# Kernel tuning notes

Measured on AMD Instinct MI355X. Metric: run time of the kernel, lower is better.

The kernel has to match this reference:

```python
import jax, jax.numpy as jnp
import numpy as np


def setup_inputs() -> dict:
    key = jax.random.key(0)
    k_xyz, k_w1, k_b1, k_w2, k_b2 = jax.random.split(key, 5)
    B, N = 2, 1024
    D_MODEL, N_HEADS = 128, 8
    HID = D_MODEL // 2
    # Kaiming-ish init scale for the tiny MLP weights
    return {
        "xyz": jax.random.normal(k_xyz, (B, 3, N), dtype=jnp.float32),
        "W1": jax.random.normal(k_w1, (3, HID), dtype=jnp.float32) * (1.0 / np.sqrt(3.0)),
        "b1": jax.random.normal(k_b1, (HID,), dtype=jnp.float32) * 0.01,
        "W2": jax.random.normal(k_w2, (HID, N_HEADS), dtype=jnp.float32) * (1.0 / np.sqrt(HID)),
        "b2": jax.random.normal(k_b2, (N_HEADS,), dtype=jnp.float32) * 0.01,
    }


def reference(xyz, W1, b1, W2, b2):
    # xyz: [B, 3, N] -> [B, N, 3]
    pts = jnp.transpose(xyz, (0, 2, 1))
    # pairwise relative positions: rel[b, i, j, :] = pts[b, j] - pts[b, i]
    # (matches xyz.unsqueeze(1) - xyz.unsqueeze(2) in torch)
    rel = pts[:, None, :, :] - pts[:, :, None, :]          # [B, N, N, 3]
    h = jax.nn.relu(jnp.einsum("bijc,ch->bijh", rel, W1) + b1)  # [B, N, N, HID]
    bias = jnp.einsum("bijh,hk->bijk", h, W2) + b2         # [B, N, N, H]
    # permute(0, 3, 1, 2) -> [B, H, N, N]
    return jnp.transpose(bias, (0, 3, 1, 2))
```

## Files before the change

kernel.cpp:

```cpp
#include <hip/hip_runtime.h>

#define HID   64
#define NHD   8
#define IT    8
#define IGRP  4
#define WAVES 8
#define JTW   32
#define JT    (WAVES*JTW)

typedef _Float16 f16x8 __attribute__((ext_vector_type(8)));
typedef float    f32x4 __attribute__((ext_vector_type(4)));

__global__ __launch_bounds__(WAVES * 64, 4) void relposenc_occ2(
    const float* __restrict__ xyz, const float* __restrict__ W1,
    const float* __restrict__ b1,  const float* __restrict__ W2,
    const float* __restrict__ b2,  float* __restrict__ out, int N) {

  __shared__ float    sW1b1[4][HID];
  __shared__ _Float16 sU[IT][HID];

  const int tid  = threadIdx.x;
  const int wave = tid >> 6;
  const int lane = tid & 63;
  const int col  = lane & 15;
  const int hgrp = lane >> 4;
  const int b    = blockIdx.z;
  const int i0   = blockIdx.y * IT;
  const int j0   = blockIdx.x * JT + wave * JTW;

  const float* xb = xyz + (size_t)b * 3 * N;

  if (tid < 4 * HID) {
    int r = tid >> 6, h = tid & 63;
    sW1b1[r][h] = (r < 3) ? W1[r * HID + h] : b1[h];
  }
  if (tid < IT * HID) {
    int ii = tid >> 6, h = tid & 63;
    int i  = i0 + ii;
    float u = fmaf(xb[i], W1[h],
              fmaf(xb[N + i], W1[HID + h],
                   xb[2 * N + i] * W1[2 * HID + h]));
    sU[ii][h] = (_Float16)u;
  }

  f16x8 aLo[2], aHi[2];
  #pragma unroll
  for (int kb = 0; kb < 2; ++kb)
    #pragma unroll
    for (int e = 0; e < 8; ++e) {
      int h = kb * 32 + hgrp * 8 + e;
      aLo[kb][e] = (_Float16)((col < NHD)  ? W2[h * NHD + col]       : 0.f);
      aHi[kb][e] = (_Float16)((col >= NHD) ? W2[h * NHD + (col - 8)] : 0.f);
    }
  float b2v[4];
  #pragma unroll
  for (int r = 0; r < 4; ++r) b2v[r] = b2[((hgrp & 1) << 2) + r];

  __syncthreads();

  f16x8 aj[2][2];
  #pragma unroll
  for (int t = 0; t < 2; ++t) {
    int j = j0 + t * 16 + col;
    float x0 = xb[j], x1 = xb[N + j], x2 = xb[2 * N + j];
    #pragma unroll
    for (int kb = 0; kb < 2; ++kb)
      #pragma unroll
      for (int e = 0; e < 8; ++e) {
        int h = kb * 32 + hgrp * 8 + e;
        float v = fmaf(x0, sW1b1[0][h],
                  fmaf(x1, sW1b1[1][h],
                  fmaf(x2, sW1b1[2][h], sW1b1[3][h])));
        aj[t][kb][e] = (_Float16)v;
      }
  }

  const size_t jj = (size_t)j0 + col + ((size_t)(lane >> 5) << 4);
  const int kbase = (hgrp & 1) << 2;
  const size_t baseOff = ((size_t)(b * NHD + kbase) * N + i0) * N + jj;
  const size_t plane = (size_t)N * N;

  const f16x8 z = {0, 0, 0, 0, 0, 0, 0, 0};

  for (int ig = 0; ig < IT; ig += IGRP) {
    f32x4 vals[IGRP];

    #pragma unroll
    for (int q = 0; q < IGRP; ++q) {
      f16x8 u0 = *(const f16x8*)&sU[ig + q][hgrp * 8];
      f16x8 u1 = *(const f16x8*)&sU[ig + q][32 + hgrp * 8];

      f16x8 d00 = __builtin_elementwise_max(aj[0][0] - u0, z);
      f16x8 d01 = __builtin_elementwise_max(aj[0][1] - u1, z);
      f16x8 d10 = __builtin_elementwise_max(aj[1][0] - u0, z);
      f16x8 d11 = __builtin_elementwise_max(aj[1][1] - u1, z);

      f32x4 cA = {b2v[0], b2v[1], b2v[2], b2v[3]};
      f32x4 cB = {0.f, 0.f, 0.f, 0.f};
      cA = __builtin_amdgcn_mfma_f32_16x16x32_f16(aLo[0], d00, cA, 0, 0, 0);
      cA = __builtin_amdgcn_mfma_f32_16x16x32_f16(aLo[1], d01, cA, 0, 0, 0);
      cB = __builtin_amdgcn_mfma_f32_16x16x32_f16(aHi[0], d10, cB, 0, 0, 0);
      cB = __builtin_amdgcn_mfma_f32_16x16x32_f16(aHi[1], d11, cB, 0, 0, 0);
      vals[q] = cA + cB;
    }

    #pragma unroll
    for (int r = 0; r < 4; ++r) {
      const size_t po = baseOff + (size_t)r * plane + (size_t)ig * N;
      #pragma unroll
      for (int q = 0; q < IGRP; ++q)
        out[po + (size_t)q * N] = vals[q][r];
    }
  }
}

extern "C" void kernel_launch(void* const* d_in, const int* in_sizes, int n_in,
                              void* d_out, int out_size, void* d_ws, size_t ws_size,
                              hipStream_t stream) {
  const float* xyz = (const float*)d_in[0];
  const float* W1  = (const float*)d_in[1];
  const float* b1  = (const float*)d_in[2];
  const float* W2  = (const float*)d_in[3];
  const float* b2  = (const float*)d_in[4];
  float* out = (float*)d_out;

  const long long in0 = in_sizes[0];
  const int N = (int)((3LL * (long long)out_size) / (8LL * in0));
  const int B = (int)(in0 / (3LL * N));

  dim3 grid(N / JT, N / IT, B);
  relposenc_occ2<<<grid, WAVES * 64, 0, stream>>>(xyz, W1, b1, W2, b2, out, N);
}
```

Before: 25.45 us.

## Precompute per-point W1 projections in a prep kernel and shrink main tiles

Adds a prep kernel that computes the per-point first-layer projections u and u+b1 as fp16, plus a transposed fp16 W2, and stores them in workspace. The main kernel then loads these vectors directly instead of recomputing them per block through shared memory and a barrier. Block size drops from 8 to 4 waves and the i-tile from 8 to 4 rows, giving more, smaller blocks. The cost is a second kernel launch and a global round-trip for the precomputed data.

Result: slower. 32.33 us (+27.0%).

```diff
diff --git a/kernel.cpp b/kernel.cpp
--- a/kernel.cpp
+++ b/kernel.cpp
@@ -2,22 +2,52 @@
 
 #define HID   64
 #define NHD   8
-#define IT    8
-#define IGRP  4
-#define WAVES 8
+#define IT    4
+#define WAVES 4
 #define JTW   32
 #define JT    (WAVES*JTW)
 
 typedef _Float16 f16x8 __attribute__((ext_vector_type(8)));
 typedef float    f32x4 __attribute__((ext_vector_type(4)));
 
-__global__ __launch_bounds__(WAVES * 64, 4) void relposenc_occ2(
+__global__ __launch_bounds__(256) void relpos_prep(
     const float* __restrict__ xyz, const float* __restrict__ W1,
     const float* __restrict__ b1,  const float* __restrict__ W2,
-    const float* __restrict__ b2,  float* __restrict__ out, int N) {
+    _Float16* __restrict__ u_all, _Float16* __restrict__ a_all,
+    _Float16* __restrict__ w2t, int N, int BN) {
+  const int tid = threadIdx.x;
+  if (blockIdx.x == 0) {
+    for (int t = tid; t < NHD * HID; t += 256) {
+      int k = t >> 6, h = t & 63;
+      w2t[k * HID + h] = (_Float16)W2[h * NHD + k];
+    }
+  }
+  int g = blockIdx.x * 256 + tid;
+  if (g >= BN) return;
+  int b = g / N, n = g - b * N;
+  const float* xb = xyz + (size_t)b * 3 * N;
+  float x0 = xb[n], x1 = xb[N + n], x2 = xb[2 * N + n];
+  _Float16* up = u_all + (size_t)g * HID;
+  _Float16* ap = a_all + (size_t)g * HID;
+  #pragma unroll
+  for (int c = 0; c < 8; ++c) {
+    f16x8 uu, aa;
+    #pragma unroll
+    for (int e = 0; e < 8; ++e) {
+      int h = c * 8 + e;
+      float u = fmaf(x0, W1[h], fmaf(x1, W1[HID + h], x2 * W1[2 * HID + h]));
+      uu[e] = (_Float16)u;
+      aa[e] = (_Float16)(u + b1[h]);
+    }
+    *(f16x8*)(up + c * 8) = uu;
+    *(f16x8*)(ap + c * 8) = aa;
+  }
+}
 
-  __shared__ float    sW1b1[4][HID];
-  __shared__ _Float16 sU[IT][HID];
+__global__ __launch_bounds__(WAVES * 64, 4) void relpos_main(
+    const _Float16* __restrict__ u_all, const _Float16* __restrict__ a_all,
+    const _Float16* __restrict__ w2t,   const float* __restrict__ b2,
+    float* __restrict__ out, int N) {
 
   const int tid  = threadIdx.x;
   const int wave = tid >> 6;
@@ -28,89 +58,64 @@
   const int i0   = blockIdx.y * IT;
   const int j0   = blockIdx.x * JT + wave * JTW;
 
-  const float* xb = xyz + (size_t)b * 3 * N;
-
-  if (tid < 4 * HID) {
-    int r = tid >> 6, h = tid & 63;
-    sW1b1[r][h] = (r < 3) ? W1[r * HID + h] : b1[h];
-  }
-  if (tid < IT * HID) {
-    int ii = tid >> 6, h = tid & 63;
-    int i  = i0 + ii;
-    float u = fmaf(xb[i], W1[h],
-              fmaf(xb[N + i], W1[HID + h],
-                   xb[2 * N + i] * W1[2 * HID + h]));
-    sU[ii][h] = (_Float16)u;
-  }
+  const f16x8 z = {0, 0, 0, 0, 0, 0, 0, 0};
 
   f16x8 aLo[2], aHi[2];
   #pragma unroll
-  for (int kb = 0; kb < 2; ++kb)
-    #pragma unroll
-    for (int e = 0; e < 8; ++e) {
-      int h = kb * 32 + hgrp * 8 + e;
-      aLo[kb][e] = (_Float16)((col < NHD)  ? W2[h * NHD + col]       : 0.f);
-      aHi[kb][e] = (_Float16)((col >= NHD) ? W2[h * NHD + (col - 8)] : 0.f);
-    }
-  float b2v[4];
-  #pragma unroll
-  for (int r = 0; r < 4; ++r) b2v[r] = b2[((hgrp & 1) << 2) + r];
-
-  __syncthreads();
+  for (int kb = 0; kb < 2; ++kb) {
+    f16x8 w = *(const f16x8*)(w2t + (col & 7) * HID + kb * 32 + hgrp * 8);
+    aLo[kb] = (col < NHD) ? w : z;
+    aHi[kb] = (col >= NHD) ? w : z;
+  }
 
   f16x8 aj[2][2];
   #pragma unroll
   for (int t = 0; t < 2; ++t) {
-    int j = j0 + t * 16 + col;
-    float x0 = xb[j], x1 = xb[N + j], x2 = xb[2 * N + j];
-    #pragma unroll
-    for (int kb = 0; kb < 2; ++kb)
-      #pragma unroll
-      for (int e = 0; e < 8; ++e) {
-        int h = kb * 32 + hgrp * 8 + e;
-        float v = fmaf(x0, sW1b1[0][h],
-                  fmaf(x1, sW1b1[1][h],
-                  fmaf(x2, sW1b1[2][h], sW1b1[3][h])));
-        aj[t][kb][e] = (_Float16)v;
-      }
+    const _Float16* ap = a_all + ((size_t)(b * N + j0 + t * 16 + col)) * HID + hgrp * 8;
+    aj[t][0] = *(const f16x8*)ap;
+    aj[t][1] = *(const f16x8*)(ap + 32);
   }
 
+  f16x8 uf[IT][2];
+  #pragma unroll
+  for (int ii = 0; ii < IT; ++ii) {
+    const _Float16* up = u_all + ((size_t)(b * N + i0 + ii)) * HID + hgrp * 8;
+    uf[ii][0] = *(const f16x8*)up;
+    uf[ii][1] = *(const f16x8*)(up + 32);
+  }
+
+  const int kbase = (hgrp & 1) << 2;
+  float b2v[4];
+  #pragma unroll
+  for (int r = 0; r < 4; ++r) b2v[r] = b2[kbase + r];
+
   const size_t jj = (size_t)j0 + col + ((size_t)(lane >> 5) << 4);
-  const int kbase = (hgrp & 1) << 2;
   const size_t baseOff = ((size_t)(b * NHD + kbase) * N + i0) * N + jj;
   const size_t plane = (size_t)N * N;
 
-  const f16x8 z = {0, 0, 0, 0, 0, 0, 0, 0};
+  f32x4 vals[IT];
+  #pragma unroll
+  for (int q = 0; q < IT; ++q) {
+    f16x8 d00 = __builtin_elementwise_max(aj[0][0] - uf[q][0], z);
+    f16x8 d01 = __builtin_elementwise_max(aj[0][1] - uf[q][1], z);
+    f16x8 d10 = __builtin_elementwise_max(aj[1][0] - uf[q][0], z);
+    f16x8 d11 = __builtin_elementwise_max(aj[1][1] - uf[q][1], z);
 
-  for (int ig = 0; ig < IT; ig += IGRP) {
-    f32x4 vals[IGRP];
+    f32x4 cA = {b2v[0], b2v[1], b2v[2], b2v[3]};
+    f32x4 cB = {0.f, 0.f, 0.f, 0.f};
+    cA = __builtin_amdgcn_mfma_f32_16x16x32_f16(aLo[0], d00, cA, 0, 0, 0);
+    cA = __builtin_amdgcn_mfma_f32_16x16x32_f16(aLo[1], d01, cA, 0, 0, 0);
+    cB = __builtin_amdgcn_mfma_f32_16x16x32_f16(aHi[0], d10, cB, 0, 0, 0);
+    cB = __builtin_amdgcn_mfma_f32_16x16x32_f16(aHi[1], d11, cB, 0, 0, 0);
+    vals[q] = cA + cB;
+  }
 
+  #pragma unroll
+  for (int r = 0; r < 4; ++r) {
+    const size_t po = baseOff + (size_t)r * plane;
     #pragma unroll
-    for (int q = 0; q < IGRP; ++q) {
-      f16x8 u0 = *(const f16x8*)&sU[ig + q][hgrp * 8];
-      f16x8 u1 = *(const f16x8*)&sU[ig + q][32 + hgrp * 8];
-
-      f16x8 d00 = __builtin_elementwise_max(aj[0][0] - u0, z);
-      f16x8 d01 = __builtin_elementwise_max(aj[0][1] - u1, z);
-      f16x8 d10 = __builtin_elementwise_max(aj[1][0] - u0, z);
-      f16x8 d11 = __builtin_elementwise_max(aj[1][1] - u1, z);
-
-      f32x4 cA = {b2v[0], b2v[1], b2v[2], b2v[3]};
-      f32x4 cB = {0.f, 0.f, 0.f, 0.f};
-      cA = __builtin_amdgcn_mfma_f32_16x16x32_f16(aLo[0], d00, cA, 0, 0, 0);
-      cA = __builtin_amdgcn_mfma_f32_16x16x32_f16(aLo[1], d01, cA, 0, 0, 0);
-      cB = __builtin_amdgcn_mfma_f32_16x16x32_f16(aHi[0], d10, cB, 0, 0, 0);
-      cB = __builtin_amdgcn_mfma_f32_16x16x32_f16(aHi[1], d11, cB, 0, 0, 0);
-      vals[q] = cA + cB;
-    }
-
-    #pragma unroll
-    for (int r = 0; r < 4; ++r) {
-      const size_t po = baseOff + (size_t)r * plane + (size_t)ig * N;
-      #pragma unroll
-      for (int q = 0; q < IGRP; ++q)
-        out[po + (size_t)q * N] = vals[q][r];
-    }
+    for (int q = 0; q < IT; ++q)
+      out[po + (size_t)q * N] = vals[q][r];
   }
 }
 
@@ -127,7 +132,15 @@
   const long long in0 = in_sizes[0];
   const int N = (int)((3LL * (long long)out_size) / (8LL * in0));
   const int B = (int)(in0 / (3LL * N));
+  const int BN = B * N;
+
+  _Float16* u_all = (_Float16*)d_ws;
+  _Float16* a_all = (_Float16*)((char*)d_ws + (size_t)BN * HID * 2);
+  _Float16* w2t   = (_Float16*)((char*)d_ws + (size_t)BN * HID * 4);
+
+  relpos_prep<<<(BN + 255) / 256, 256, 0, stream>>>(
+      xyz, W1, b1, W2, u_all, a_all, w2t, N, BN);
 
   dim3 grid(N / JT, N / IT, B);
-  relposenc_occ2<<<grid, WAVES * 64, 0, stream>>>(xyz, W1, b1, W2, b2, out, N);
+  relpos_main<<<grid, WAVES * 64, 0, stream>>>(u_all, a_all, w2t, b2, out, N);
 }
```
